# Performance work log

Hardware: AMD Instinct MI355X
Metric: run time of the kernel (lower is better)

Reference implementation:

```python
import jax, jax.numpy as jnp
import numpy as np


def setup_inputs() -> dict:
    key = jax.random.key(0)
    ks = jax.random.split(key, 8)
    B, N, F = 16, 2048, 128
    x = jax.random.normal(ks[0], (B, N, F), dtype=jnp.float32)
    # dense (pre-normalized) adjacency, as spektral GCNConv expects normalized A
    a = jax.random.uniform(ks[1], (B, N, N), dtype=jnp.float32) / N
    w1 = jax.random.normal(ks[2], (F, 32), dtype=jnp.float32) * 0.1
    b1 = jnp.zeros((32,), dtype=jnp.float32)
    w2 = jax.random.normal(ks[3], (32, 32), dtype=jnp.float32) * 0.1
    b2 = jnp.zeros((32,), dtype=jnp.float32)
    wf1 = jax.random.normal(ks[4], (32, 512), dtype=jnp.float32) * 0.1
    bf1 = jnp.zeros((512,), dtype=jnp.float32)
    wf2 = jax.random.normal(ks[5], (512, 1), dtype=jnp.float32) * 0.1
    bf2 = jnp.zeros((1,), dtype=jnp.float32)
    return {"x": x, "a": a, "w1": w1, "b1": b1, "w2": w2, "b2": b2,
            "wf1": wf1, "bf1": bf1, "wf2": wf2, "bf2": bf2}


def _gcn(x, a, w, b):
    # GCNConv: elu(A_norm @ X @ W + b)
    h = jnp.einsum('bnf,fc->bnc', x, w)   # dense transform first (cheaper)
    h = jnp.einsum('bnm,bmc->bnc', a, h)  # adjacency aggregation
    return jax.nn.elu(h + b)


def reference(x, a, w1, b1, w2, b2, wf1, bf1, wf2, bf2):
    h = _gcn(x, a, w1, b1)                # [B,N,32]
    h = _gcn(h, a, w2, b2)                # [B,N,32]
    pooled = jnp.sum(h, axis=1)           # GlobalSumPool -> [B,32]
    h = jax.nn.relu(pooled @ wf1 + bf1)   # [B,512]
    out = jax.nn.sigmoid(h @ wf2 + bf2)   # [B,1]
    return out
```

## Files before the change

kernel.cpp:

```cpp
#include <hip/hip_runtime.h>
#include <hip/hip_bf16.h>
#include <math.h>

#define BATCH 16
#define NN 2048
#define FF 128
#define CC 32
#define HID 512
#define QM 512
#define LSTR 520
#define KS1 128

typedef float v4f __attribute__((ext_vector_type(4)));
typedef float v2f __attribute__((ext_vector_type(2)));
typedef short short8 __attribute__((ext_vector_type(8)));
typedef short s4v __attribute__((ext_vector_type(4)));

__device__ __forceinline__ unsigned short f2bf(float f) {
  unsigned u = __float_as_uint(f);
  u += 0x7fffu + ((u >> 16) & 1u);
  return (unsigned short)(u >> 16);
}

__device__ __forceinline__ float elu1(float x) {
  return x > 0.f ? x : expm1f(x);
}

__global__ __launch_bounds__(256)
void k_xw1(const float* __restrict__ src, const float* __restrict__ w,
           unsigned short* __restrict__ outT) {
  int t = threadIdx.x;
  int wv = t >> 6, l = t & 63, lo = l & 15, q = l >> 4;
  int rowt = blockIdx.x * 4 + wv;
  long row = (long)rowt * 16 + lo;

  short8 wf[FF / 32][2];
#pragma unroll
  for (int kc = 0; kc < FF / 32; ++kc)
#pragma unroll
    for (int h = 0; h < 2; ++h) {
      short8 f;
#pragma unroll
      for (int j = 0; j < 8; ++j)
        f[j] = (short)f2bf(w[(kc * 32 + q * 8 + j) * CC + h * 16 + lo]);
      wf[kc][h] = f;
    }

  v4f acc0 = {0.f, 0.f, 0.f, 0.f}, acc1 = {0.f, 0.f, 0.f, 0.f};
#pragma unroll
  for (int kc = 0; kc < FF / 32; ++kc) {
    const float* sp = src + row * FF + kc * 32 + q * 8;
    float4 a0 = *(const float4*)sp;
    float4 a1 = *(const float4*)(sp + 4);
    short8 af;
    af[0] = (short)f2bf(a0.x); af[1] = (short)f2bf(a0.y);
    af[2] = (short)f2bf(a0.z); af[3] = (short)f2bf(a0.w);
    af[4] = (short)f2bf(a1.x); af[5] = (short)f2bf(a1.y);
    af[6] = (short)f2bf(a1.z); af[7] = (short)f2bf(a1.w);
    acc0 = __builtin_amdgcn_mfma_f32_16x16x32_bf16(af, wf[kc][0], acc0, 0, 0, 0);
    acc1 = __builtin_amdgcn_mfma_f32_16x16x32_bf16(af, wf[kc][1], acc1, 0, 0, 0);
  }

  int b = rowt >> 7;
  int nbase = (rowt & 127) * 16;
#pragma unroll
  for (int r = 0; r < 4; ++r) {
    int n = nbase + q * 4 + r;
    outT[((long)b * CC + lo) * NN + n] = f2bf(acc0[r]);
    outT[((long)b * CC + 16 + lo) * NN + n] = f2bf(acc1[r]);
  }
}

__global__ __launch_bounds__(256, 2)
void k_agg1f(const float* __restrict__ a, unsigned char* __restrict__ afp8,
             const unsigned short* __restrict__ hT, const float* __restrict__ b1,
             float* __restrict__ h1) {
  __shared__ __attribute__((aligned(16))) unsigned short hs[CC * LSTR];
  __shared__ __attribute__((aligned(16))) unsigned short at[2][64 * KS1];

  int t = threadIdx.x;
  int bid = blockIdx.x;
  int rt = bid & 31, b = bid >> 5;
  int n0 = rt * 64;

  int r0 = t >> 5, chunk = t & 31;
  const float* ga = a + ((long)(b * NN + n0 + r0)) * NN + chunk * 4;
  unsigned char* gao = afp8 + ((long)(b * NN + n0 + r0)) * NN + chunk * 4;
  int swb = r0 * 256 + ((chunk * 8) ^ (r0 << 4));

  float4 ar[8];
  const float sc = 1024.f;

#pragma unroll
  for (int j = 0; j < 8; ++j)
    ar[j] = *(const float4*)(ga + (long)j * 8 * NN);

#pragma unroll
  for (int i = 0; i < 8; ++i) {
    int jj = i * 256 + t;
    int c = jj >> 6, off = (jj & 63) * 8;
    *(uint4*)&hs[c * LSTR + off] =
        *(const uint4*)(hT + ((long)b * CC + c) * NN + off);
  }

#pragma unroll
  for (int j = 0; j < 8; ++j) {
    char* lp = (char*)&at[0][0] + swb + j * 2048;
    s4v bv;
    bv[0] = (short)f2bf(ar[j].x); bv[1] = (short)f2bf(ar[j].y);
    bv[2] = (short)f2bf(ar[j].z); bv[3] = (short)f2bf(ar[j].w);
    *(s4v*)lp = bv;
    int w0 = __builtin_amdgcn_cvt_pk_fp8_f32(ar[j].x * sc, ar[j].y * sc, 0, false);
    w0 = __builtin_amdgcn_cvt_pk_fp8_f32(ar[j].z * sc, ar[j].w * sc, w0, true);
    *(int*)(gao + (long)j * 8 * NN) = w0;
  }
  __syncthreads();

  int l = t & 63, wv = t >> 6, lo = l & 15, q = l >> 4;
  int lrow = wv * 16 + lo;
  const unsigned short* h0 = &hs[lo * LSTR + q * 8];

  v4f acc0 = {0.f, 0.f, 0.f, 0.f}, acc1 = {0.f, 0.f, 0.f, 0.f};

  for (int step = 0; step < 16; ++step) {
    if (step < 15) {
#pragma unroll
      for (int j = 0; j < 8; ++j)
        ar[j] = *(const float4*)(ga + (long)j * 8 * NN + (step + 1) * KS1);
    }
    const char* ab = (const char*)at + (step & 1) * (64 * KS1 * 2);
    int mloc = (step & 3) * KS1;
#pragma unroll
    for (int kk = 0; kk < 4; ++kk) {
      short8 af = *(const short8*)(ab + lrow * 256 +
                                   ((q * 16 + kk * 64) ^ ((lo & 7) << 4)));
      int m = mloc + kk * 32;
      short8 b0 = *(const short8*)(h0 + m);
      short8 b1v = *(const short8*)(h0 + 16 * LSTR + m);
      acc0 = __builtin_amdgcn_mfma_f32_16x16x32_bf16(af, b0, acc0, 0, 0, 0);
      acc1 = __builtin_amdgcn_mfma_f32_16x16x32_bf16(af, b1v, acc1, 0, 0, 0);
    }
    if (step < 15) {
      char* lb = (char*)&at[(step + 1) & 1][0];
#pragma unroll
      for (int j = 0; j < 8; ++j) {
        char* lp = lb + swb + j * 2048;
        s4v bv;
        bv[0] = (short)f2bf(ar[j].x); bv[1] = (short)f2bf(ar[j].y);
        bv[2] = (short)f2bf(ar[j].z); bv[3] = (short)f2bf(ar[j].w);
        *(s4v*)lp = bv;
        int w0 = __builtin_amdgcn_cvt_pk_fp8_f32(ar[j].x * sc, ar[j].y * sc, 0, false);
        w0 = __builtin_amdgcn_cvt_pk_fp8_f32(ar[j].z * sc, ar[j].w * sc, w0, true);
        *(int*)(gao + (long)j * 8 * NN + (step + 1) * KS1) = w0;
      }
      __syncthreads();
      if ((step & 3) == 3) {
        int qm = (step >> 2) + 1;
#pragma unroll
        for (int i = 0; i < 8; ++i) {
          int jj = i * 256 + t;
          int c = jj >> 6, off = (jj & 63) * 8;
          *(uint4*)&hs[c * LSTR + off] =
              *(const uint4*)(hT + ((long)b * CC + c) * NN + qm * QM + off);
        }
        __syncthreads();
      }
    }
  }

  float* hp = h1 + (long)b * NN * CC;
#pragma unroll
  for (int r = 0; r < 4; ++r) {
    int n = n0 + wv * 16 + q * 4 + r;
    hp[(long)n * CC + lo] = elu1(acc0[r] + b1[lo]);
    hp[(long)n * CC + 16 + lo] = elu1(acc1[r] + b1[16 + lo]);
  }
}

__global__ __launch_bounds__(256)
void k_xw2(const float* __restrict__ h1, const float* __restrict__ w2,
           unsigned short* __restrict__ outT) {
  int t = threadIdx.x;
  int wv = t >> 6, l = t & 63, lo = l & 15, q = l >> 4;
  int rowt = blockIdx.x * 4 + wv;
  long row = (long)rowt * 16 + lo;

  short8 wf[2];
#pragma unroll
  for (int h = 0; h < 2; ++h) {
    short8 f;
#pragma unroll
    for (int j = 0; j < 8; ++j)
      f[j] = (short)f2bf(w2[(q * 8 + j) * CC + h * 16 + lo]);
    wf[h] = f;
  }

  const float* p = h1 + row * CC + q * 8;
  float4 u0 = *(const float4*)p;
  float4 u1 = *(const float4*)(p + 4);
  short8 af;
  af[0] = (short)f2bf(u0.x); af[1] = (short)f2bf(u0.y);
  af[2] = (short)f2bf(u0.z); af[3] = (short)f2bf(u0.w);
  af[4] = (short)f2bf(u1.x); af[5] = (short)f2bf(u1.y);
  af[6] = (short)f2bf(u1.z); af[7] = (short)f2bf(u1.w);

  v4f acc0 = {0.f, 0.f, 0.f, 0.f}, acc1 = {0.f, 0.f, 0.f, 0.f};
  acc0 = __builtin_amdgcn_mfma_f32_16x16x32_bf16(af, wf[0], acc0, 0, 0, 0);
  acc1 = __builtin_amdgcn_mfma_f32_16x16x32_bf16(af, wf[1], acc1, 0, 0, 0);

  const float inv = 1.f / 1024.f;
  int b = rowt >> 7;
  int nbase = (rowt & 127) * 16;
#pragma unroll
  for (int r = 0; r < 4; ++r) {
    int n = nbase + q * 4 + r;
    outT[((long)b * CC + lo) * NN + n] = f2bf(acc0[r] * inv);
    outT[((long)b * CC + 16 + lo) * NN + n] = f2bf(acc1[r] * inv);
  }
}

__global__ __launch_bounds__(256, 2)
void k_agg2f(const unsigned char* __restrict__ afp8,
             const unsigned short* __restrict__ hT, const float* __restrict__ b2,
             float* __restrict__ pp2) {
  __shared__ __attribute__((aligned(16))) unsigned short hs[CC * LSTR];
  __shared__ __attribute__((aligned(16))) unsigned char a2[64 * QM];
  __shared__ float red[4][CC];

  int t = threadIdx.x;
  int bid = blockIdx.x;
  int rt = bid & 31, b = bid >> 5;
  int n0 = rt * 64;

  int r0 = t >> 5, chunk = t & 31;
  const unsigned char* ga = afp8 + ((long)(b * NN + n0 + r0)) * NN + chunk * 16;
  char* lw = (char*)a2 + r0 * 512 + ((chunk * 16) ^ (r0 << 4));

  uint4 arr[8];
#pragma unroll
  for (int j = 0; j < 8; ++j)
    arr[j] = *(const uint4*)(ga + (long)j * 8 * NN);
#pragma unroll
  for (int i = 0; i < 8; ++i) {
    int jj = i * 256 + t;
    int c = jj >> 6, off = (jj & 63) * 8;
    *(uint4*)&hs[c * LSTR + off] =
        *(const uint4*)(hT + ((long)b * CC + c) * NN + off);
  }
#pragma unroll
  for (int j = 0; j < 8; ++j)
    *(uint4*)(lw + j * 4096) = arr[j];
  __syncthreads();

  int l = t & 63, wv = t >> 6, lo = l & 15, q = l >> 4;
  int lrow = wv * 16 + lo;
  const unsigned short* h0 = &hs[lo * LSTR + q * 8];
  const char* ab = (const char*)a2;

  v4f acc0 = {0.f, 0.f, 0.f, 0.f}, acc1 = {0.f, 0.f, 0.f, 0.f};

  for (int qm = 0; qm < 4; ++qm) {
    if (qm < 3) {
#pragma unroll
      for (int j = 0; j < 8; ++j)
        arr[j] = *(const uint4*)(ga + (long)j * 8 * NN + (qm + 1) * QM);
    }
#pragma unroll
    for (int kk = 0; kk < 16; ++kk) {
      int2 av = *(const int2*)(ab + lrow * 512 +
                               ((q * 8 + kk * 32) ^ ((lo & 7) << 4)));
      v2f f01 = __builtin_amdgcn_cvt_pk_f32_fp8(av.x, false);
      v2f f23 = __builtin_amdgcn_cvt_pk_f32_fp8(av.x, true);
      v2f f45 = __builtin_amdgcn_cvt_pk_f32_fp8(av.y, false);
      v2f f67 = __builtin_amdgcn_cvt_pk_f32_fp8(av.y, true);
      short8 af;
      af[0] = (short)f2bf(f01.x); af[1] = (short)f2bf(f01.y);
      af[2] = (short)f2bf(f23.x); af[3] = (short)f2bf(f23.y);
      af[4] = (short)f2bf(f45.x); af[5] = (short)f2bf(f45.y);
      af[6] = (short)f2bf(f67.x); af[7] = (short)f2bf(f67.y);
      int m = kk * 32;
      short8 b0 = *(const short8*)(h0 + m);
      short8 b1v = *(const short8*)(h0 + 16 * LSTR + m);
      acc0 = __builtin_amdgcn_mfma_f32_16x16x32_bf16(af, b0, acc0, 0, 0, 0);
      acc1 = __builtin_amdgcn_mfma_f32_16x16x32_bf16(af, b1v, acc1, 0, 0, 0);
    }
    if (qm < 3) {
      __syncthreads();
#pragma unroll
      for (int j = 0; j < 8; ++j)
        *(uint4*)(lw + j * 4096) = arr[j];
      int nq = qm + 1;
#pragma unroll
      for (int i = 0; i < 8; ++i) {
        int jj = i * 256 + t;
        int c = jj >> 6, off = (jj & 63) * 8;
        *(uint4*)&hs[c * LSTR + off] =
            *(const uint4*)(hT + ((long)b * CC + c) * NN + nq * QM + off);
      }
      __syncthreads();
    }
  }

  float s0 = 0.f, s1 = 0.f;
  float bc0 = b2[lo], bc1 = b2[16 + lo];
#pragma unroll
  for (int r = 0; r < 4; ++r) {
    s0 += elu1(acc0[r] + bc0);
    s1 += elu1(acc1[r] + bc1);
  }
  s0 += __shfl_xor(s0, 16); s0 += __shfl_xor(s0, 32);
  s1 += __shfl_xor(s1, 16); s1 += __shfl_xor(s1, 32);
  if (l < 16) {
    red[wv][lo] = s0;
    red[wv][16 + lo] = s1;
  }
  __syncthreads();
  if (t < CC) {
    float p = red[0][t] + red[1][t] + red[2][t] + red[3][t];
    pp2[((long)b * 32 + rt) * CC + t] = p;
  }
}

__global__ __launch_bounds__(512)
void k5_mlp(const float* __restrict__ pp2, const float* __restrict__ wf1,
            const float* __restrict__ bf1, const float* __restrict__ wf2,
            const float* __restrict__ bf2, float* __restrict__ out) {
  __shared__ float red[HID];
  __shared__ float ps[CC];
  int b = blockIdx.x, j = threadIdx.x;
  if (j < CC) {
    float s = 0.f;
#pragma unroll
    for (int rt = 0; rt < 32; ++rt) s += pp2[((long)b * 32 + rt) * CC + j];
    ps[j] = s;
  }
  __syncthreads();
  float acc = bf1[j];
#pragma unroll
  for (int c = 0; c < CC; ++c) acc += ps[c] * wf1[c * HID + j];
  red[j] = fmaxf(acc, 0.f) * wf2[j];
  __syncthreads();
  for (int s = HID / 2; s > 0; s >>= 1) {
    if (j < s) red[j] += red[j + s];
    __syncthreads();
  }
  if (j == 0) out[b] = 1.f / (1.f + expf(-(red[0] + bf2[0])));
}

extern "C" void kernel_launch(void* const* d_in, const int* in_sizes, int n_in,
                              void* d_out, int out_size, void* d_ws, size_t ws_size,
                              hipStream_t stream) {
  const float* x   = (const float*)d_in[0];
  const float* a   = (const float*)d_in[1];
  const float* w1  = (const float*)d_in[2];
  const float* b1  = (const float*)d_in[3];
  const float* w2  = (const float*)d_in[4];
  const float* b2  = (const float*)d_in[5];
  const float* wf1 = (const float*)d_in[6];
  const float* bf1 = (const float*)d_in[7];
  const float* wf2 = (const float*)d_in[8];
  const float* bf2 = (const float*)d_in[9];
  float* out = (float*)d_out;

  char* ws = (char*)d_ws;
  unsigned char*  afp8 = (unsigned char*)ws;
  unsigned short* hT1  = (unsigned short*)(ws + 0x4000000UL);
  unsigned short* hT2  = (unsigned short*)(ws + 0x4200000UL);
  float* h1  = (float*)(ws + 0x4400000UL);
  float* pp2 = (float*)(ws + 0x4800000UL);

  k_xw1<<<512, 256, 0, stream>>>(x, w1, hT1);
  k_agg1f<<<512, 256, 0, stream>>>(a, afp8, hT1, b1, h1);
  k_xw2<<<512, 256, 0, stream>>>(h1, w2, hT2);
  k_agg2f<<<512, 256, 0, stream>>>(afp8, hT2, b2, pp2);
  k5_mlp<<<BATCH, HID, 0, stream>>>(pp2, wf1, bf1, wf2, bf2, out);
}
```

Baseline: 438.1 us.

## Fuse second feature transform into first aggregation and double block width

```diff
diff --git a/kernel.cpp b/kernel.cpp
--- a/kernel.cpp
+++ b/kernel.cpp
@@ -9,7 +9,7 @@
 #define HID 512
 #define QM 512
 #define LSTR 520
-#define KS1 128
+#define KS2 256
 
 typedef float v4f __attribute__((ext_vector_type(4)));
 typedef float v2f __attribute__((ext_vector_type(2)));
@@ -71,22 +71,22 @@
   }
 }
 
-__global__ __launch_bounds__(256, 2)
+__global__ __launch_bounds__(512, 4)
 void k_agg1f(const float* __restrict__ a, unsigned char* __restrict__ afp8,
              const unsigned short* __restrict__ hT, const float* __restrict__ b1,
-             float* __restrict__ h1) {
+             const float* __restrict__ w2, unsigned short* __restrict__ hT2out) {
   __shared__ __attribute__((aligned(16))) unsigned short hs[CC * LSTR];
-  __shared__ __attribute__((aligned(16))) unsigned short at[2][64 * KS1];
+  __shared__ __attribute__((aligned(16))) unsigned short at[64 * KS2];
 
   int t = threadIdx.x;
   int bid = blockIdx.x;
   int rt = bid & 31, b = bid >> 5;
   int n0 = rt * 64;
 
-  int r0 = t >> 5, chunk = t & 31;
+  int r0 = t >> 6, chunk = t & 63;
   const float* ga = a + ((long)(b * NN + n0 + r0)) * NN + chunk * 4;
   unsigned char* gao = afp8 + ((long)(b * NN + n0 + r0)) * NN + chunk * 4;
-  int swb = r0 * 256 + ((chunk * 8) ^ (r0 << 4));
+  int swb = r0 * 512 + ((chunk * 8) ^ (r0 << 4));
 
   float4 ar[8];
   const float sc = 1024.f;
@@ -96,8 +96,8 @@
     ar[j] = *(const float4*)(ga + (long)j * 8 * NN);
 
 #pragma unroll
-  for (int i = 0; i < 8; ++i) {
-    int jj = i * 256 + t;
+  for (int i = 0; i < 4; ++i) {
+    int jj = i * 512 + t;
     int c = jj >> 6, off = (jj & 63) * 8;
     *(uint4*)&hs[c * LSTR + off] =
         *(const uint4*)(hT + ((long)b * CC + c) * NN + off);
@@ -105,7 +105,7 @@
 
 #pragma unroll
   for (int j = 0; j < 8; ++j) {
-    char* lp = (char*)&at[0][0] + swb + j * 2048;
+    char* lp = (char*)at + swb + j * 4096;
     s4v bv;
     bv[0] = (short)f2bf(ar[j].x); bv[1] = (short)f2bf(ar[j].y);
     bv[2] = (short)f2bf(ar[j].z); bv[3] = (short)f2bf(ar[j].w);
@@ -116,158 +116,144 @@
   }
   __syncthreads();
 
-  int l = t & 63, wv = t >> 6, lo = l & 15, q = l >> 4;
-  int lrow = wv * 16 + lo;
-  const unsigned short* h0 = &hs[lo * LSTR + q * 8];
-
-  v4f acc0 = {0.f, 0.f, 0.f, 0.f}, acc1 = {0.f, 0.f, 0.f, 0.f};
-
-  for (int step = 0; step < 16; ++step) {
-    if (step < 15) {
+  int wv = t >> 6, l = t & 63, lo = l & 15, q = l >> 4;
+  int tile = wv & 3, half = wv >> 2;
+  int lrow = tile * 16 + lo;
+  const unsigned short* h0 = &hs[(half * 16 + lo) * LSTR + q * 8];
+
+  v4f acc = {0.f, 0.f, 0.f, 0.f};
+
+  for (int step = 0; step < 8; ++step) {
+    uint4 hreg[4];
+    if (step < 7) {
 #pragma unroll
       for (int j = 0; j < 8; ++j)
-        ar[j] = *(const float4*)(ga + (long)j * 8 * NN + (step + 1) * KS1);
-    }
-    const char* ab = (const char*)at + (step & 1) * (64 * KS1 * 2);
-    int mloc = (step & 3) * KS1;
-#pragma unroll
-    for (int kk = 0; kk < 4; ++kk) {
-      short8 af = *(const short8*)(ab + lrow * 256 +
+        ar[j] = *(const float4*)(ga + (long)j * 8 * NN + (step + 1) * KS2);
+      if (step & 1) {
+        int qm = (step + 1) >> 1;
+#pragma unroll
+        for (int i = 0; i < 4; ++i) {
+          int jj = i * 512 + t;
+          int c = jj >> 6, off = (jj & 63) * 8;
+          hreg[i] = *(const uint4*)(hT + ((long)b * CC + c) * NN + qm * QM + off);
+        }
+      }
+    }
+    int mloc = (step & 1) * KS2;
+#pragma unroll
+    for (int kk = 0; kk < 8; ++kk) {
+      short8 af = *(const short8*)((const char*)at + lrow * 512 +
                                    ((q * 16 + kk * 64) ^ ((lo & 7) << 4)));
-      int m = mloc + kk * 32;
-      short8 b0 = *(const short8*)(h0 + m);
-      short8 b1v = *(const short8*)(h0 + 16 * LSTR + m);
-      acc0 = __builtin_amdgcn_mfma_f32_16x16x32_bf16(af, b0, acc0, 0, 0, 0);
-      acc1 = __builtin_amdgcn_mfma_f32_16x16x32_bf16(af, b1v, acc1, 0, 0, 0);
-    }
-    if (step < 15) {
-      char* lb = (char*)&at[(step + 1) & 1][0];
+      short8 bf = *(const short8*)(h0 + mloc + kk * 32);
+      acc = __builtin_amdgcn_mfma_f32_16x16x32_bf16(af, bf, acc, 0, 0, 0);
+    }
+    if (step < 7) {
+      __syncthreads();
 #pragma unroll
       for (int j = 0; j < 8; ++j) {
-        char* lp = lb + swb + j * 2048;
+        char* lp = (char*)at + swb + j * 4096;
         s4v bv;
         bv[0] = (short)f2bf(ar[j].x); bv[1] = (short)f2bf(ar[j].y);
         bv[2] = (short)f2bf(ar[j].z); bv[3] = (short)f2bf(ar[j].w);
         *(s4v*)lp = bv;
         int w0 = __builtin_amdgcn_cvt_pk_fp8_f32(ar[j].x * sc, ar[j].y * sc, 0, false);
         w0 = __builtin_amdgcn_cvt_pk_fp8_f32(ar[j].z * sc, ar[j].w * sc, w0, true);
-        *(int*)(gao + (long)j * 8 * NN + (step + 1) * KS1) = w0;
+        *(int*)(gao + (long)j * 8 * NN + (step + 1) * KS2) = w0;
+      }
+      if (step & 1) {
+#pragma unroll
+        for (int i = 0; i < 4; ++i) {
+          int jj = i * 512 + t;
+          int c = jj >> 6, off = (jj & 63) * 8;
+          *(uint4*)&hs[c * LSTR + off] = hreg[i];
+        }
       }
       __syncthreads();
-      if ((step & 3) == 3) {
-        int qm = (step >> 2) + 1;
-#pragma unroll
-        for (int i = 0; i < 8; ++i) {
-          int jj = i * 256 + t;
-          int c = jj >> 6, off = (jj & 63) * 8;
-          *(uint4*)&hs[c * LSTR + off] =
-              *(const uint4*)(hT + ((long)b * CC + c) * NN + qm * QM + off);
-        }
-        __syncthreads();
-      }
-    }
-  }
-
-  float* hp = h1 + (long)b * NN * CC;
+    }
+  }
+
+  __syncthreads();
+  float* hrow = (float*)hs;
+  float bc = b1[half * 16 + lo];
+#pragma unroll
+  for (int r = 0; r < 4; ++r)
+    hrow[(tile * 16 + q * 4 + r) * 33 + half * 16 + lo] = elu1(acc[r] + bc);
+  __syncthreads();
+
+  short8 wf, af;
+#pragma unroll
+  for (int j = 0; j < 8; ++j) {
+    wf[j] = (short)f2bf(w2[(q * 8 + j) * CC + half * 16 + lo]);
+    af[j] = (short)f2bf(hrow[(tile * 16 + lo) * 33 + q * 8 + j]);
+  }
+  v4f acc2 = {0.f, 0.f, 0.f, 0.f};
+  acc2 = __builtin_amdgcn_mfma_f32_16x16x32_bf16(af, wf, acc2, 0, 0, 0);
+
+  const float inv = 1.f / 1024.f;
 #pragma unroll
   for (int r = 0; r < 4; ++r) {
-    int n = n0 + wv * 16 + q * 4 + r;
-    hp[(long)n * CC + lo] = elu1(acc0[r] + b1[lo]);
-    hp[(long)n * CC + 16 + lo] = elu1(acc1[r] + b1[16 + lo]);
-  }
-}
-
-__global__ __launch_bounds__(256)
-void k_xw2(const float* __restrict__ h1, const float* __restrict__ w2,
-           unsigned short* __restrict__ outT) {
-  int t = threadIdx.x;
-  int wv = t >> 6, l = t & 63, lo = l & 15, q = l >> 4;
-  int rowt = blockIdx.x * 4 + wv;
-  long row = (long)rowt * 16 + lo;
-
-  short8 wf[2];
-#pragma unroll
-  for (int h = 0; h < 2; ++h) {
-    short8 f;
-#pragma unroll
-    for (int j = 0; j < 8; ++j)
-      f[j] = (short)f2bf(w2[(q * 8 + j) * CC + h * 16 + lo]);
-    wf[h] = f;
-  }
-
-  const float* p = h1 + row * CC + q * 8;
-  float4 u0 = *(const float4*)p;
-  float4 u1 = *(const float4*)(p + 4);
-  short8 af;
-  af[0] = (short)f2bf(u0.x); af[1] = (short)f2bf(u0.y);
-  af[2] = (short)f2bf(u0.z); af[3] = (short)f2bf(u0.w);
-  af[4] = (short)f2bf(u1.x); af[5] = (short)f2bf(u1.y);
-  af[6] = (short)f2bf(u1.z); af[7] = (short)f2bf(u1.w);
-
-  v4f acc0 = {0.f, 0.f, 0.f, 0.f}, acc1 = {0.f, 0.f, 0.f, 0.f};
-  acc0 = __builtin_amdgcn_mfma_f32_16x16x32_bf16(af, wf[0], acc0, 0, 0, 0);
-  acc1 = __builtin_amdgcn_mfma_f32_16x16x32_bf16(af, wf[1], acc1, 0, 0, 0);
-
-  const float inv = 1.f / 1024.f;
-  int b = rowt >> 7;
-  int nbase = (rowt & 127) * 16;
-#pragma unroll
-  for (int r = 0; r < 4; ++r) {
-    int n = nbase + q * 4 + r;
-    outT[((long)b * CC + lo) * NN + n] = f2bf(acc0[r] * inv);
-    outT[((long)b * CC + 16 + lo) * NN + n] = f2bf(acc1[r] * inv);
-  }
-}
-
-__global__ __launch_bounds__(256, 2)
+    int n = n0 + tile * 16 + q * 4 + r;
+    hT2out[((long)b * CC + half * 16 + lo) * NN + n] = f2bf(acc2[r] * inv);
+  }
+}
+
+__global__ __launch_bounds__(512, 4)
 void k_agg2f(const unsigned char* __restrict__ afp8,
              const unsigned short* __restrict__ hT, const float* __restrict__ b2,
              float* __restrict__ pp2) {
   __shared__ __attribute__((aligned(16))) unsigned short hs[CC * LSTR];
   __shared__ __attribute__((aligned(16))) unsigned char a2[64 * QM];
-  __shared__ float red[4][CC];
+  __shared__ float red[8][16];
 
   int t = threadIdx.x;
   int bid = blockIdx.x;
   int rt = bid & 31, b = bid >> 5;
   int n0 = rt * 64;
 
-  int r0 = t >> 5, chunk = t & 31;
-  const unsigned char* ga = afp8 + ((long)(b * NN + n0 + r0)) * NN + chunk * 16;
-  char* lw = (char*)a2 + r0 * 512 + ((chunk * 16) ^ (r0 << 4));
-
-  uint4 arr[8];
-#pragma unroll
-  for (int j = 0; j < 8; ++j)
-    arr[j] = *(const uint4*)(ga + (long)j * 8 * NN);
-#pragma unroll
-  for (int i = 0; i < 8; ++i) {
-    int jj = i * 256 + t;
+  int rr = t >> 5, chunk = t & 31;
+  const unsigned char* ga = afp8 + ((long)(b * NN + n0 + rr)) * NN + chunk * 16;
+  char* lw = (char*)a2 + rr * 512 + ((chunk * 16) ^ ((rr & 7) << 4));
+
+  uint4 arr[4];
+#pragma unroll
+  for (int j = 0; j < 4; ++j)
+    arr[j] = *(const uint4*)(ga + (long)j * 16 * NN);
+#pragma unroll
+  for (int i = 0; i < 4; ++i) {
+    int jj = i * 512 + t;
     int c = jj >> 6, off = (jj & 63) * 8;
     *(uint4*)&hs[c * LSTR + off] =
         *(const uint4*)(hT + ((long)b * CC + c) * NN + off);
   }
 #pragma unroll
-  for (int j = 0; j < 8; ++j)
-    *(uint4*)(lw + j * 4096) = arr[j];
-  __syncthreads();
-
-  int l = t & 63, wv = t >> 6, lo = l & 15, q = l >> 4;
-  int lrow = wv * 16 + lo;
-  const unsigned short* h0 = &hs[lo * LSTR + q * 8];
-  const char* ab = (const char*)a2;
-
-  v4f acc0 = {0.f, 0.f, 0.f, 0.f}, acc1 = {0.f, 0.f, 0.f, 0.f};
+  for (int j = 0; j < 4; ++j)
+    *(uint4*)(lw + j * 8192) = arr[j];
+  __syncthreads();
+
+  int wv = t >> 6, l = t & 63, lo = l & 15, q = l >> 4;
+  int tile = wv & 3, half = wv >> 2;
+  int lrow = tile * 16 + lo;
+  const unsigned short* h0 = &hs[(half * 16 + lo) * LSTR + q * 8];
+
+  v4f acc = {0.f, 0.f, 0.f, 0.f};
 
   for (int qm = 0; qm < 4; ++qm) {
+    uint4 hreg[4];
     if (qm < 3) {
 #pragma unroll
-      for (int j = 0; j < 8; ++j)
-        arr[j] = *(const uint4*)(ga + (long)j * 8 * NN + (qm + 1) * QM);
+      for (int j = 0; j < 4; ++j)
+        arr[j] = *(const uint4*)(ga + (long)j * 16 * NN + (qm + 1) * QM);
+#pragma unroll
+      for (int i = 0; i < 4; ++i) {
+        int jj = i * 512 + t;
+        int c = jj >> 6, off = (jj & 63) * 8;
+        hreg[i] = *(const uint4*)(hT + ((long)b * CC + c) * NN +
+                                  (qm + 1) * QM + off);
+      }
     }
 #pragma unroll
     for (int kk = 0; kk < 16; ++kk) {
-      int2 av = *(const int2*)(ab + lrow * 512 +
+      int2 av = *(const int2*)((const char*)a2 + lrow * 512 +
                                ((q * 8 + kk * 32) ^ ((lo & 7) << 4)));
       v2f f01 = __builtin_amdgcn_cvt_pk_f32_fp8(av.x, false);
       v2f f23 = __builtin_amdgcn_cvt_pk_f32_fp8(av.x, true);
@@ -278,45 +264,36 @@
       af[2] = (short)f2bf(f23.x); af[3] = (short)f2bf(f23.y);
       af[4] = (short)f2bf(f45.x); af[5] = (short)f2bf(f45.y);
       af[6] = (short)f2bf(f67.x); af[7] = (short)f2bf(f67.y);
-      int m = kk * 32;
-      short8 b0 = *(const short8*)(h0 + m);
-      short8 b1v = *(const short8*)(h0 + 16 * LSTR + m);
-      acc0 = __builtin_amdgcn_mfma_f32_16x16x32_bf16(af, b0, acc0, 0, 0, 0);
-      acc1 = __builtin_amdgcn_mfma_f32_16x16x32_bf16(af, b1v, acc1, 0, 0, 0);
+      short8 bf = *(const short8*)(h0 + kk * 32);
+      acc = __builtin_amdgcn_mfma_f32_16x16x32_bf16(af, bf, acc, 0, 0, 0);
     }
     if (qm < 3) {
       __syncthreads();
 #pragma unroll
-      for (int j = 0; j < 8; ++j)
-        *(uint4*)(lw + j * 4096) = arr[j];
-      int nq = qm + 1;
-#pragma unroll
-      for (int i = 0; i < 8; ++i) {
-        int jj = i * 256 + t;
+      for (int j = 0; j < 4; ++j)
+        *(uint4*)(lw + j * 8192) = arr[j];
+#pragma unroll
+      for (int i = 0; i < 4; ++i) {
+        int jj = i * 512 + t;
         int c = jj >> 6, off = (jj & 63) * 8;
-        *(uint4*)&hs[c * LSTR + off] =
-            *(const uint4*)(hT + ((long)b * CC + c) * NN + nq * QM + off);
+        *(uint4*)&hs[c * LSTR + off] = hreg[i];
       }
       __syncthreads();
     }
   }
 
-  float s0 = 0.f, s1 = 0.f;
-  float bc0 = b2[lo], bc1 = b2[16 + lo];
-#pragma unroll
-  for (int r = 0; r < 4; ++r) {
-    s0 += elu1(acc0[r] + bc0);
-    s1 += elu1(acc1[r] + bc1);
-  }
-  s0 += __shfl_xor(s0, 16); s0 += __shfl_xor(s0, 32);
-  s1 += __shfl_xor(s1, 16); s1 += __shfl_xor(s1, 32);
-  if (l < 16) {
-    red[wv][lo] = s0;
-    red[wv][16 + lo] = s1;
-  }
+  float bc = b2[half * 16 + lo];
+  float s = 0.f;
+#pragma unroll
+  for (int r = 0; r < 4; ++r) s += elu1(acc[r] + bc);
+  s += __shfl_xor(s, 16);
+  s += __shfl_xor(s, 32);
+  if (l < 16) red[wv][lo] = s;
   __syncthreads();
   if (t < CC) {
-    float p = red[0][t] + red[1][t] + red[2][t] + red[3][t];
+    int h = t >> 4, c = t & 15;
+    float p = red[h * 4 + 0][c] + red[h * 4 + 1][c] +
+              red[h * 4 + 2][c] + red[h * 4 + 3][c];
     pp2[((long)b * 32 + rt) * CC + t] = p;
   }
 }
@@ -366,12 +343,10 @@
   unsigned char*  afp8 = (unsigned char*)ws;
   unsigned short* hT1  = (unsigned short*)(ws + 0x4000000UL);
   unsigned short* hT2  = (unsigned short*)(ws + 0x4200000UL);
-  float* h1  = (float*)(ws + 0x4400000UL);
-  float* pp2 = (float*)(ws + 0x4800000UL);
+  float* pp2 = (float*)(ws + 0x4400000UL);
 
   k_xw1<<<512, 256, 0, stream>>>(x, w1, hT1);
-  k_agg1f<<<512, 256, 0, stream>>>(a, afp8, hT1, b1, h1);
-  k_xw2<<<512, 256, 0, stream>>>(h1, w2, hT2);
-  k_agg2f<<<512, 256, 0, stream>>>(afp8, hT2, b2, pp2);
+  k_agg1f<<<512, 512, 0, stream>>>(a, afp8, hT1, b1, w2, hT2);
+  k_agg2f<<<512, 512, 0, stream>>>(afp8, hT2, b2, pp2);
   k5_mlp<<<BATCH, HID, 0, stream>>>(pp2, wf1, bf1, wf2, bf2, out);
 }
```

Result: slower. 452.6 us (+3.3%).
